# Kernel tuning notes

Hardware: AMD Instinct MI355X
Metric: run time of the kernel (lower is better)

Reference implementation:

```python
import jax, jax.numpy as jnp
import numpy as np
from jax import lax

B, T, HID, H, DK, DV, K = 2, 2048, 1024, 16, 64, 64, 4
SCALE = float(DK) ** -0.5
EPS = 1e-5


def setup_inputs() -> dict:
    key = jax.random.key(0)
    ks = jax.random.split(key, 12)
    n = lambda k, sh, s=0.02: (jax.random.normal(k, sh, jnp.float32) * s)
    return {
        "x": jax.random.normal(ks[0], (B, T, HID), jnp.float32),
        "Wq": n(ks[1], (H * DK, HID)),
        "Wk": n(ks[2], (H * DK, HID)),
        "Wv": n(ks[3], (H * DV, HID)),
        "Wa": n(ks[4], (H * DV, HID)), "ba": jnp.zeros((H * DV,), jnp.float32),
        "Wb": n(ks[5], (H, HID)), "bb": jnp.zeros((H,), jnp.float32),
        "Wg": n(ks[6], (H * DV, HID)),
        "Wo": n(ks[7], (HID, H * DV)),
        "qcw": n(ks[8], (H * DK, 1, K), 0.3), "qcb": jnp.zeros((H * DK,), jnp.float32),
        "kcw": n(ks[9], (H * DK, 1, K), 0.3), "kcb": jnp.zeros((H * DK,), jnp.float32),
        "vcw": n(ks[10], (H * DV, 1, K), 0.3), "vcb": jnp.zeros((H * DV,), jnp.float32),
        "ln_w": jnp.ones((DV,), jnp.float32), "ln_b": jnp.zeros((DV,), jnp.float32),
    }


def _causal_dwconv_silu(z, w, b):
    # z: [B,T,C], w: [C,1,K] depthwise. Conv1d(padding=K-1) then slice[:T] == causal left-pad.
    zc = z.transpose(0, 2, 1)  # [B,C,T]
    y = lax.conv_general_dilated(zc, w, (1,), [(K - 1, 0)],
                                 dimension_numbers=("NCH", "OIH", "NCH"),
                                 feature_group_count=zc.shape[1])
    return jax.nn.silu((y + b[None, :, None]).transpose(0, 2, 1))


def reference(x, Wq, Wk, Wv, Wa, ba, Wb, bb, Wg, Wo,
              qcw, qcb, kcw, kcb, vcw, vcb, ln_w, ln_b):
    Bb, Tt, _ = x.shape
    q = _causal_dwconv_silu(x @ Wq.T, qcw, qcb).reshape(Bb, Tt, H, DK)
    k = _causal_dwconv_silu(x @ Wk.T, kcw, kcb).reshape(Bb, Tt, H, DK) * SCALE
    v = _causal_dwconv_silu(x @ Wv.T, vcw, vcb).reshape(Bb, Tt, H, DV)
    a = jax.nn.sigmoid(x @ Wa.T + ba).reshape(Bb, Tt, H, DV)
    beta = jax.nn.sigmoid(x @ Wb.T + bb)  # [B,T,H]

    def step(S, inp):
        qt, kt, vt, at, bt = inp  # qt/kt: [B,H,DK], vt/at: [B,H,DV], bt: [B,H]
        err = jnp.einsum("bhij,bhj->bhi", S, kt) - vt          # S@k - v
        S = at[..., None] * S - bt[..., None, None] * (err[..., None] * kt[:, :, None, :])
        o = jnp.einsum("bhij,bhj->bhi", S, qt)                 # S@q
        return S, o

    xs = tuple(jnp.moveaxis(t, 1, 0) for t in (q, k, v, a, beta))  # time-leading
    S0 = jnp.zeros((Bb, H, DV, DK), x.dtype)
    _, o = lax.scan(step, S0, xs)
    o = jnp.moveaxis(o, 0, 1)  # [B,T,H,DV]

    mu = o.mean(-1, keepdims=True)
    var = ((o - mu) ** 2).mean(-1, keepdims=True)
    o = (o - mu) / jnp.sqrt(var + EPS) * ln_w + ln_b

    g = jax.nn.sigmoid(x @ Wg.T).reshape(Bb, Tt, H, DV)
    o = (o * g).reshape(Bb, Tt, H * DV)
    return o @ Wo.T
```

## Files before the change

### kernel.cpp

```cpp
#include <hip/hip_runtime.h>
#include <hip/hip_bf16.h>
#include <cstdint>


using bf16 = __hip_bfloat16;
typedef __bf16 bf16x8 __attribute__((ext_vector_type(8)));
typedef __bf16 bf16x4v __attribute__((ext_vector_type(4)));
typedef float f32x4 __attribute__((ext_vector_type(4)));
typedef float f32x2 __attribute__((ext_vector_type(2)));
typedef unsigned int u32x4 __attribute__((ext_vector_type(4)));
typedef unsigned int u32x2 __attribute__((ext_vector_type(2)));

__device__ __forceinline__ __bf16 cvt_bf16(float f) {
  __hip_bfloat16 h = (__hip_bfloat16)f;
  return *reinterpret_cast<__bf16*>(&h);
}
__device__ __forceinline__ void async_copy16(const void* g, void* l) {
  __builtin_amdgcn_global_load_lds((const __attribute__((address_space(1))) void*)g,
                                   (__attribute__((address_space(3))) void*)l,
                                   16, 0, 0);
}
__device__ __forceinline__ float bcf(unsigned int u) { return __builtin_bit_cast(float, u); }
template <int CTRL>
__device__ __forceinline__ float dpp_f(float x) {
  int y = __builtin_amdgcn_update_dpp(0, __builtin_bit_cast(int, x), CTRL, 0xF, 0xF, true);
  return __builtin_bit_cast(float, y);
}

__global__ __launch_bounds__(256) void cvtw_kernel(
    const float* __restrict__ x, const float* __restrict__ Wq,
    const float* __restrict__ Wk, const float* __restrict__ Wv,
    const float* __restrict__ Wa, const float* __restrict__ Wg,
    const float* __restrict__ Wo, bf16* __restrict__ xb,
    bf16* __restrict__ w4b, bf16* __restrict__ wgb, bf16* __restrict__ wob)
{
  int blk = blockIdx.x;
  const float* src;
  __bf16* dst;
  size_t off;
  if (blk < 4096) {
    src = x; dst = (__bf16*)xb;
    off = (size_t)blk * 1024 + threadIdx.x * 4;
  } else if (blk < 8192) {
    int wb = blk - 4096;
    int wi = wb >> 10;
    src = (wi == 0) ? Wq : (wi == 1) ? Wk : (wi == 2) ? Wv : Wa;
    dst = (__bf16*)w4b + (size_t)wi * 1024 * 1024;
    off = (size_t)(wb & 1023) * 1024 + threadIdx.x * 4;
  } else if (blk < 9216) {
    src = Wg; dst = (__bf16*)wgb;
    off = (size_t)(blk - 8192) * 1024 + threadIdx.x * 4;
  } else {
    src = Wo; dst = (__bf16*)wob;
    off = (size_t)(blk - 9216) * 1024 + threadIdx.x * 4;
  }
  float4 f = *(const float4*)(src + off);
  bf16x4v t;
  t[0] = cvt_bf16(f.x); t[1] = cvt_bf16(f.y); t[2] = cvt_bf16(f.z); t[3] = cvt_bf16(f.w);
  *(bf16x4v*)(dst + off) = t;
}

template <int MODE, bool A_FP32>
__global__ __launch_bounds__(256) void gemm_bt(
    const void* __restrict__ Av, const float* __restrict__ Bt,
    const float* __restrict__ bias, float* __restrict__ Cf, bf16* __restrict__ Cb,
    int M, int N, int K)
{
  __shared__ __align__(16) __bf16 As[128 * 32];
  __shared__ __align__(16) __bf16 Bs[128 * 32];

  const int tid  = threadIdx.x;
  const int lane = tid & 63;
  const int wave = tid >> 6;
  const int tile_m = blockIdx.y * 128;
  const int tile_n = blockIdx.x * 128;
  const int wm = (wave >> 1) * 64;
  const int wn = (wave & 1) * 64;

  const int srow = lane >> 2;
  const int scol = (lane & 3) * 8;

  f32x4 acc[4][4];
#pragma unroll
  for (int i = 0; i < 4; ++i)
#pragma unroll
    for (int j = 0; j < 4; ++j) acc[i][j] = {0.f, 0.f, 0.f, 0.f};

  for (int k0 = 0; k0 < K; k0 += 32) {
    float4 b0[2], b1[2], a0[2], a1[2];
#pragma unroll
    for (int s = 0; s < 2; ++s) {
      int brow = tile_n + s * 64 + wave * 16 + srow;
      if (brow > N - 1) brow = N - 1;
      const float* bp = Bt + (size_t)brow * K + k0 + scol;
      b0[s] = *(const float4*)bp;
      b1[s] = *(const float4*)(bp + 4);
      if (A_FP32) {
        int arow = tile_m + s * 64 + wave * 16 + srow;
        const float* ap = (const float*)Av + (size_t)arow * K + k0 + scol;
        a0[s] = *(const float4*)ap;
        a1[s] = *(const float4*)(ap + 4);
      }
    }
    __syncthreads();
#pragma unroll
    for (int s = 0; s < 2; ++s) {
      if (!A_FP32) {
        int arow = tile_m + s * 64 + wave * 16 + srow;
        async_copy16((const __bf16*)Av + (size_t)arow * K + k0 + scol,
                     &As[(s * 64 + wave * 16 + srow) * 32 + scol]);
      } else {
        bf16x8 ua;
        ua[0] = cvt_bf16(a0[s].x); ua[1] = cvt_bf16(a0[s].y);
        ua[2] = cvt_bf16(a0[s].z); ua[3] = cvt_bf16(a0[s].w);
        ua[4] = cvt_bf16(a1[s].x); ua[5] = cvt_bf16(a1[s].y);
        ua[6] = cvt_bf16(a1[s].z); ua[7] = cvt_bf16(a1[s].w);
        *(bf16x8*)&As[(s * 64 + wave * 16 + srow) * 32 + scol] = ua;
      }
      bf16x8 u;
      u[0] = cvt_bf16(b0[s].x); u[1] = cvt_bf16(b0[s].y);
      u[2] = cvt_bf16(b0[s].z); u[3] = cvt_bf16(b0[s].w);
      u[4] = cvt_bf16(b1[s].x); u[5] = cvt_bf16(b1[s].y);
      u[6] = cvt_bf16(b1[s].z); u[7] = cvt_bf16(b1[s].w);
      *(bf16x8*)&Bs[(s * 64 + wave * 16 + srow) * 32 + scol] = u;
    }
    __syncthreads();

    bf16x8 af[4], bfr[4];
#pragma unroll
    for (int i = 0; i < 4; ++i)
      af[i] = *(const bf16x8*)&As[(wm + i * 16 + (lane & 15)) * 32 + (lane >> 4) * 8];
#pragma unroll
    for (int j = 0; j < 4; ++j)
      bfr[j] = *(const bf16x8*)&Bs[(wn + j * 16 + (lane & 15)) * 32 + (lane >> 4) * 8];

#pragma unroll
    for (int i = 0; i < 4; ++i)
#pragma unroll
      for (int j = 0; j < 4; ++j)
        acc[i][j] = __builtin_amdgcn_mfma_f32_16x16x32_bf16(af[i], bfr[j], acc[i][j], 0, 0, 0);
  }

#pragma unroll
  for (int i = 0; i < 4; ++i) {
#pragma unroll
    for (int j = 0; j < 4; ++j) {
#pragma unroll
      for (int r = 0; r < 4; ++r) {
        int gm = tile_m + wm + i * 16 + (lane >> 4) * 4 + r;
        int gn = tile_n + wn + j * 16 + (lane & 15);
        if (gn < N) {
          float val = acc[i][j][r];
          if (MODE == 3 || MODE == 5) {
            float bv = bias ? bias[gn] : 0.f;
            val = 1.f / (1.f + __expf(-(val + bv)));
          }
          if (MODE == 4)      Cf[(size_t)gm * N + gn] = val;
          else if (MODE == 5) Cf[(size_t)gn * M + gm] = val;
          else                Cb[(size_t)gm * N + gn] = (bf16)val;
        }
      }
    }
  }
}

__global__ __launch_bounds__(256) void gemm_bb(
    const bf16* __restrict__ A, const bf16* __restrict__ Bw,
    float* __restrict__ C)
{
  __shared__ __align__(16) __bf16 As[128 * 32];
  __shared__ __align__(16) __bf16 Bs[128 * 32];

  const int tid  = threadIdx.x;
  const int lane = tid & 63;
  const int wave = tid >> 6;
  const int tile_m = blockIdx.y * 128;
  const int tile_n = blockIdx.x * 128;
  const int wm = (wave >> 1) * 64;
  const int wn = (wave & 1) * 64;
  const int srow = lane >> 2;
  const int scol = (lane & 3) * 8;

  f32x4 acc[4][4];
#pragma unroll
  for (int i = 0; i < 4; ++i)
#pragma unroll
    for (int j = 0; j < 4; ++j) acc[i][j] = {0.f, 0.f, 0.f, 0.f};

  for (int k0 = 0; k0 < 1024; k0 += 32) {
    __syncthreads();
#pragma unroll
    for (int s = 0; s < 2; ++s) {
      int arow = tile_m + s * 64 + wave * 16 + srow;
      async_copy16((const __bf16*)A + (size_t)arow * 1024 + k0 + scol,
                   &As[(s * 64 + wave * 16 + srow) * 32 + scol]);
      int brow = tile_n + s * 64 + wave * 16 + srow;
      async_copy16((const __bf16*)Bw + (size_t)brow * 1024 + k0 + scol,
                   &Bs[(s * 64 + wave * 16 + srow) * 32 + scol]);
    }
    __syncthreads();

    bf16x8 af[4], bfr[4];
#pragma unroll
    for (int i = 0; i < 4; ++i)
      af[i] = *(const bf16x8*)&As[(wm + i * 16 + (lane & 15)) * 32 + (lane >> 4) * 8];
#pragma unroll
    for (int j = 0; j < 4; ++j)
      bfr[j] = *(const bf16x8*)&Bs[(wn + j * 16 + (lane & 15)) * 32 + (lane >> 4) * 8];

#pragma unroll
    for (int i = 0; i < 4; ++i)
#pragma unroll
      for (int j = 0; j < 4; ++j)
        acc[i][j] = __builtin_amdgcn_mfma_f32_16x16x32_bf16(af[i], bfr[j], acc[i][j], 0, 0, 0);
  }

#pragma unroll
  for (int i = 0; i < 4; ++i)
#pragma unroll
    for (int j = 0; j < 4; ++j)
#pragma unroll
      for (int r = 0; r < 4; ++r) {
        int gm = tile_m + wm + i * 16 + (lane >> 4) * 4 + r;
        int gn = tile_n + wn + j * 16 + (lane & 15);
        C[(size_t)gm * 1024 + gn] = acc[i][j][r];
      }
}

__global__ __launch_bounds__(256) void mega_gemm2(
    const bf16* __restrict__ Av, const bf16* __restrict__ W4b,
    const float* __restrict__ Wb, const float* __restrict__ bb,
    const float* __restrict__ ba, bf16* __restrict__ C4,
    float* __restrict__ betab)
{
  __shared__ __align__(16) __bf16 As[128 * 32];
  __shared__ __align__(16) __bf16 Bs[128 * 32];

  const int tid  = threadIdx.x;
  const int lane = tid & 63;
  const int wave = tid >> 6;
  const int tile_m = blockIdx.y * 128;
  const bool isbeta = (blockIdx.x >= 32);
  const int tile_n = isbeta ? 0 : blockIdx.x * 128;
  const int grp = tile_n >> 10;
  const int tnl = tile_n & 1023;
  const int wm = (wave >> 1) * 64;
  const int wn = (wave & 1) * 64;

  const int srow = lane >> 2;
  const int scol = (lane & 3) * 8;

  f32x4 acc[4][4];
#pragma unroll
  for (int i = 0; i < 4; ++i)
#pragma unroll
    for (int j = 0; j < 4; ++j) acc[i][j] = {0.f, 0.f, 0.f, 0.f};

  const __bf16* Wp = (const __bf16*)W4b + (size_t)grp * 1024 * 1024;

  for (int k0 = 0; k0 < 1024; k0 += 32) {
    float4 b0[2], b1[2];
    if (isbeta) {
#pragma unroll
      for (int s = 0; s < 2; ++s) {
        int brow = s * 64 + wave * 16 + srow;
        if (brow > 15) brow = 15;
        const float* bp = Wb + (size_t)brow * 1024 + k0 + scol;
        b0[s] = *(const float4*)bp;
        b1[s] = *(const float4*)(bp + 4);
      }
    }
    __syncthreads();
#pragma unroll
    for (int s = 0; s < 2; ++s) {
      int arow = tile_m + s * 64 + wave * 16 + srow;
      async_copy16((const __bf16*)Av + (size_t)arow * 1024 + k0 + scol,
                   &As[(s * 64 + wave * 16 + srow) * 32 + scol]);
      if (!isbeta) {
        int brow = tnl + s * 64 + wave * 16 + srow;
        async_copy16(Wp + (size_t)brow * 1024 + k0 + scol,
                     &Bs[(s * 64 + wave * 16 + srow) * 32 + scol]);
      } else {
        bf16x8 u;
        u[0] = cvt_bf16(b0[s].x); u[1] = cvt_bf16(b0[s].y);
        u[2] = cvt_bf16(b0[s].z); u[3] = cvt_bf16(b0[s].w);
        u[4] = cvt_bf16(b1[s].x); u[5] = cvt_bf16(b1[s].y);
        u[6] = cvt_bf16(b1[s].z); u[7] = cvt_bf16(b1[s].w);
        *(bf16x8*)&Bs[(s * 64 + wave * 16 + srow) * 32 + scol] = u;
      }
    }
    __syncthreads();

    bf16x8 af[4], bfr[4];
#pragma unroll
    for (int i = 0; i < 4; ++i)
      af[i] = *(const bf16x8*)&As[(wm + i * 16 + (lane & 15)) * 32 + (lane >> 4) * 8];
#pragma unroll
    for (int j = 0; j < 4; ++j)
      bfr[j] = *(const bf16x8*)&Bs[(wn + j * 16 + (lane & 15)) * 32 + (lane >> 4) * 8];

#pragma unroll
    for (int i = 0; i < 4; ++i)
#pragma unroll
      for (int j = 0; j < 4; ++j)
        acc[i][j] = __builtin_amdgcn_mfma_f32_16x16x32_bf16(af[i], bfr[j], acc[i][j], 0, 0, 0);
  }

  if (!isbeta) {
    bf16* Cp = (bf16*)((__bf16*)C4 + (size_t)grp * 4096 * 1024);
#pragma unroll
    for (int i = 0; i < 4; ++i)
#pragma unroll
      for (int j = 0; j < 4; ++j)
#pragma unroll
        for (int r = 0; r < 4; ++r) {
          int gm = tile_m + wm + i * 16 + (lane >> 4) * 4 + r;
          int col = tnl + wn + j * 16 + (lane & 15);
          float val = acc[i][j][r];
          if (grp == 3) val = 1.f / (1.f + __expf(-(val + ba[col])));
          ((__bf16*)Cp)[(size_t)gm * 1024 + col] = cvt_bf16(val);
        }
  } else {
#pragma unroll
    for (int i = 0; i < 4; ++i)
#pragma unroll
      for (int j = 0; j < 4; ++j)
#pragma unroll
        for (int r = 0; r < 4; ++r) {
          int gm = tile_m + wm + i * 16 + (lane >> 4) * 4 + r;
          int gn = wn + j * 16 + (lane & 15);
          if (gn < 16) {
            float val = 1.f / (1.f + __expf(-(acc[i][j][r] + bb[gn])));
            betab[(size_t)gn * 4096 + gm] = val;
          }
        }
  }
}

__global__ __launch_bounds__(256) void conv_silu_kernel(
    const bf16* __restrict__ z, const float* __restrict__ w,
    const float* __restrict__ bias, bf16* __restrict__ out, float scale)
{
  int idx = blockIdx.x * 256 + threadIdx.x;
  int c8 = idx & 127;
  int m  = idx >> 7;
  int t  = m & 2047;
  int c0 = c8 * 8;

  const __bf16* base = (const __bf16*)z + (size_t)m * 1024 + c0;
  const bf16x8 zzero = __builtin_bit_cast(bf16x8, (u32x4){0u, 0u, 0u, 0u});
  bf16x8 z3 = *(const bf16x8*)base;
  bf16x8 z2 = (t >= 1) ? *(const bf16x8*)(base - 1024) : zzero;
  bf16x8 z1 = (t >= 2) ? *(const bf16x8*)(base - 2048) : zzero;
  bf16x8 z0 = (t >= 3) ? *(const bf16x8*)(base - 3072) : zzero;

  const float* wp = w + c0 * 4;
  bf16x8 res;
#pragma unroll
  for (int e = 0; e < 8; ++e) {
    float4 we = *(const float4*)(wp + e * 4);
    float acc = bias[c0 + e] + (float)z3[e] * we.w;
    acc += (float)z2[e] * we.z;
    acc += (float)z1[e] * we.y;
    acc += (float)z0[e] * we.x;
    float s = acc / (1.f + __expf(-acc));
    res[e] = cvt_bf16(s * scale);
  }
  *(bf16x8*)((__bf16*)out + (size_t)m * 1024 + c0) = res;
}

__global__ __launch_bounds__(256) void kk_kernel(
    const bf16* __restrict__ k, const float* __restrict__ betab,
    float* __restrict__ G)
{
  int tid = blockIdx.x * 256 + threadIdx.x;
  int out = tid >> 2;
  int j   = tid & 3;
  int h = out >> 12;
  int m = out & 4095;
  int t = m & 2047;
  float s = 0.f;
  if (t > 0) {
    const __bf16* r1 = (const __bf16*)k + (size_t)m * 1024 + h * 64 + j * 16;
    const __bf16* r0 = r1 - 1024;
    bf16x8 a0 = *(const bf16x8*)r0;
    bf16x8 a1 = *(const bf16x8*)(r0 + 8);
    bf16x8 b0 = *(const bf16x8*)r1;
    bf16x8 b1 = *(const bf16x8*)(r1 + 8);
#pragma unroll
    for (int e = 0; e < 8; ++e)
      s += (float)a0[e] * (float)b0[e] + (float)a1[e] * (float)b1[e];
  }
  s += __shfl_xor(s, 1);
  s += __shfl_xor(s, 2);
  if (j == 0) G[out] = betab[out] * s;
}

#define SCAN_STEP(i, KN0, KN1, Q0, Q1, WV, WA, BT, GT, LAST)                  \
  {                                                                           \
    const float vr = ((i) & 1) ? bcf((WV) & 0xffff0000u) : bcf((WV) << 16);   \
    const float ar = ((i) & 1) ? bcf((WA) & 0xffff0000u) : bcf((WA) << 16);   \
    float unxt = 0.f;                                                         \
    f32x2 k2n0 = {0.f, 0.f}, k2n1 = {0.f, 0.f};                               \
    if (!(LAST)) {                                                            \
      k2n0 = unpk(KN0); k2n1 = unpk(KN1);                                     \
      f32x2 dd = S20 * k2n0; dd += S21 * k2n1;                                \
      unxt = dd[0] + dd[1];                                                   \
      unxt += dpp_f<0xB1>(unxt);  unxt += dpp_f<0x4E>(unxt);                  \
      unxt += dpp_f<0x141>(unxt); unxt += dpp_f<0x140>(unxt);                 \
    } else { Sold0 = S20; Sold1 = S21; }                                      \
    float A_ = (BT) * __builtin_fmaf(aprev, u, -vr);                          \
    cc = __builtin_fmaf(-cc, (GT), A_);                                       \
    f32x2 q20 = unpk(Q0), q21 = unpk(Q1);                                     \
    const f32x2 cc2 = {cc, cc}, arv = {ar, ar};                               \
    f32x2 oo;                                                                 \
    { f32x2 t0 = cc2 * k2c0; S20 = arv * S20 - t0; oo = S20 * q20;            \
      f32x2 t1 = cc2 * k2c1; S21 = arv * S21 - t1; oo += S21 * q21; }         \
    so[(i)][lane] = oo[0] + oo[1];                                            \
    aprev = ar;                                                               \
    if (!(LAST)) { k2c0 = k2n0; k2c1 = k2n1; u = unxt; }                      \
  }

#define LOADG(KS, QS, VS, AS, BS, GS, g)                                      \
  KS = *(const u32x4*)&skT[buf][sg][(g) * 8];                                 \
  QS = *(const u32x4*)&sqT[buf][sg][(g) * 8];                                 \
  VS = *(const unsigned int*)&svaT[buf][0][r4][(g) * 2];                      \
  AS = *(const unsigned int*)&svaT[buf][1][r4][(g) * 2];                      \
  BS = *(const f32x2*)&sbeta[c * 16 + (g) * 2];                               \
  GS = *(const f32x2*)&sG[c * 16 + (g) * 2];

__global__ __launch_bounds__(256) void scan_gemm_kernel(
    const bf16* __restrict__ q, const bf16* __restrict__ k,
    const bf16* __restrict__ v, const bf16* __restrict__ a,
    const float* __restrict__ betab, const float* __restrict__ gkk,
    bf16* __restrict__ o,
    const float* __restrict__ x, const bf16* __restrict__ Wgb,
    bf16* __restrict__ gout)
{
  __shared__ __align__(16) __bf16 skT[2][16][72];
  __shared__ __align__(16) __bf16 sqT[2][16][72];
  __shared__ __align__(16) __bf16 svaT[2][2][4][16];
  __shared__ __align__(16) float  so[16][68];
  __shared__ __align__(16) __bf16 so2[16][4];
  __shared__ float sbeta[2048];
  __shared__ float sG[2048];
  __shared__ __align__(16) __bf16 As[128 * 32];
  __shared__ __align__(16) __bf16 Bs[128 * 32];

  if (blockIdx.x >= 512) {
    const int gb   = blockIdx.x - 512;
    const int tid  = threadIdx.x;
    const int lane = tid & 63;
    const int wave = tid >> 6;
    const int tile_m = (gb >> 3) * 128;
    const int tile_n = (gb & 7) * 128;
    const int wm = (wave >> 1) * 64;
    const int wn = (wave & 1) * 64;
    const int srow = lane >> 2;
    const int scol = (lane & 3) * 8;

    f32x4 acc[4][4];
#pragma unroll
    for (int i = 0; i < 4; ++i)
#pragma unroll
      for (int j = 0; j < 4; ++j) acc[i][j] = {0.f, 0.f, 0.f, 0.f};

    for (int k0 = 0; k0 < 1024; k0 += 32) {
      float4 a0[2], a1[2];
#pragma unroll
      for (int s = 0; s < 2; ++s) {
        int arow = tile_m + s * 64 + wave * 16 + srow;
        const float* ap = x + (size_t)arow * 1024 + k0 + scol;
        a0[s] = *(const float4*)ap;
        a1[s] = *(const float4*)(ap + 4);
      }
      __syncthreads();
#pragma unroll
      for (int s = 0; s < 2; ++s) {
        bf16x8 ua;
        ua[0] = cvt_bf16(a0[s].x); ua[1] = cvt_bf16(a0[s].y);
        ua[2] = cvt_bf16(a0[s].z); ua[3] = cvt_bf16(a0[s].w);
        ua[4] = cvt_bf16(a1[s].x); ua[5] = cvt_bf16(a1[s].y);
        ua[6] = cvt_bf16(a1[s].z); ua[7] = cvt_bf16(a1[s].w);
        *(bf16x8*)&As[(s * 64 + wave * 16 + srow) * 32 + scol] = ua;
        int brow = tile_n + s * 64 + wave * 16 + srow;
        async_copy16((const __bf16*)Wgb + (size_t)brow * 1024 + k0 + scol,
                     &Bs[(s * 64 + wave * 16 + srow) * 32 + scol]);
      }
      __syncthreads();

      bf16x8 af[4], bfr[4];
#pragma unroll
      for (int i = 0; i < 4; ++i)
        af[i] = *(const bf16x8*)&As[(wm + i * 16 + (lane & 15)) * 32 + (lane >> 4) * 8];
#pragma unroll
      for (int j = 0; j < 4; ++j)
        bfr[j] = *(const bf16x8*)&Bs[(wn + j * 16 + (lane & 15)) * 32 + (lane >> 4) * 8];

#pragma unroll
      for (int i = 0; i < 4; ++i)
#pragma unroll
        for (int j = 0; j < 4; ++j)
          acc[i][j] = __builtin_amdgcn_mfma_f32_16x16x32_bf16(af[i], bfr[j], acc[i][j], 0, 0, 0);
    }

#pragma unroll
    for (int i = 0; i < 4; ++i)
#pragma unroll
      for (int j = 0; j < 4; ++j)
#pragma unroll
        for (int r = 0; r < 4; ++r) {
          int gm = tile_m + wm + i * 16 + (lane >> 4) * 4 + r;
          int gn = tile_n + wn + j * 16 + (lane & 15);
          float val = 1.f / (1.f + __expf(-acc[i][j][r]));
          gout[(size_t)gm * 1024 + gn] = (bf16)val;
        }
    return;
  }

  if (threadIdx.x >= 64) return;

  const int blk = blockIdx.x;
  const int qd = blk >> 5;
  const int bh = blk & 31;
  const int b = bh >> 4, h = bh & 15;
  const int lane = threadIdx.x;
  const int r4 = lane >> 4;
  const int sg = lane & 15;

  {
    const float* bp = betab + (size_t)h * 4096 + b * 2048;
    const float* gp = gkk   + (size_t)h * 4096 + b * 2048;
    for (int t = lane; t < 2048; t += 64) { sbeta[t] = bp[t]; sG[t] = gp[t]; }
  }

  const size_t bkq = (size_t)b * 2048 * 1024 + h * 64;
  const size_t bva = bkq + qd * 4;
  const __bf16* kp = (const __bf16*)k;
  const __bf16* qp = (const __bf16*)q;

  const int g_st = lane >> 3;
  const int g_cg = (lane & 7) * 8;
  const int sgp  = (lane & 7) * 2;
  const int va_vh = (lane >> 4) & 1;
  const int va_st = lane & 15;

  bf16x8 pk0, pk1, pq0, pq1;
  bf16x4v pva;
  auto fetch = [&](int t0) {
    int st0 = t0 + g_st, st1 = t0 + 8 + g_st;
    pk0 = *(const bf16x8*)(kp + bkq + (size_t)st0 * 1024 + g_cg);
    pk1 = *(const bf16x8*)(kp + bkq + (size_t)st1 * 1024 + g_cg);
    pq0 = *(const bf16x8*)(qp + bkq + (size_t)st0 * 1024 + g_cg);
    pq1 = *(const bf16x8*)(qp + bkq + (size_t)st1 * 1024 + g_cg);
    if (lane < 32) {
      const __bf16* src = va_vh ? (const __bf16*)a : (const __bf16*)v;
      pva = *(const bf16x4v*)(src + bva + (size_t)(t0 + va_st) * 1024);
    }
  };
  auto commit = [&](int cb) {
    {
      u32x4 wk = __builtin_bit_cast(u32x4, pk0);
      u32x4 wq = __builtin_bit_cast(u32x4, pq0);
      u32x2 lo, hi;
      lo[0] = wk[0]; lo[1] = wk[1]; hi[0] = wk[2]; hi[1] = wk[3];
      *(u32x2*)&skT[cb][sgp][g_st * 4]     = lo;
      *(u32x2*)&skT[cb][sgp + 1][g_st * 4] = hi;
      lo[0] = wq[0]; lo[1] = wq[1]; hi[0] = wq[2]; hi[1] = wq[3];
      *(u32x2*)&sqT[cb][sgp][g_st * 4]     = lo;
      *(u32x2*)&sqT[cb][sgp + 1][g_st * 4] = hi;
    }
    {
      u32x4 wk = __builtin_bit_cast(u32x4, pk1);
      u32x4 wq = __builtin_bit_cast(u32x4, pq1);
      u32x2 lo, hi;
      lo[0] = wk[0]; lo[1] = wk[1]; hi[0] = wk[2]; hi[1] = wk[3];
      *(u32x2*)&skT[cb][sgp][(8 + g_st) * 4]     = lo;
      *(u32x2*)&skT[cb][sgp + 1][(8 + g_st) * 4] = hi;
      lo[0] = wq[0]; lo[1] = wq[1]; hi[0] = wq[2]; hi[1] = wq[3];
      *(u32x2*)&sqT[cb][sgp][(8 + g_st) * 4]     = lo;
      *(u32x2*)&sqT[cb][sgp + 1][(8 + g_st) * 4] = hi;
    }
    if (lane < 32) {
#pragma unroll
      for (int r = 0; r < 4; ++r) svaT[cb][va_vh][r][va_st] = pva[r];
    }
  };

  fetch(0); commit(0);

  f32x2 S20 = {0.f, 0.f}, S21 = {0.f, 0.f};
  f32x2 Sold0 = {0.f, 0.f}, Sold1 = {0.f, 0.f};
  float u = 0.f, cc = 0.f, aprev = 0.f;

  auto unpk = [&](unsigned int w) -> f32x2 {
    f32x2 r; r[0] = bcf(w << 16); r[1] = bcf(w & 0xffff0000u); return r;
  };

  for (int c = 0; c < 128; ++c) {
    const int buf = c & 1;
    const bool hasNext = (c + 1 < 128);

    if (hasNext) fetch((c + 1) * 16);

    u32x4 kA, qA, kB, qB, kC, qC;
    unsigned int vA, aA, vB, aB, vC, aC;
    f32x2 bA, gA, bB, gB, bC, gC;

    LOADG(kA, qA, vA, aA, bA, gA, 0)
    LOADG(kB, qB, vB, aB, bB, gB, 1)
    LOADG(kC, qC, vC, aC, bC, gC, 2)

    f32x2 k2c0 = unpk(kA[0]);
    f32x2 k2c1 = unpk(kA[1]);
    {
      f32x2 dd = Sold0 * k2c0;
      dd += Sold1 * k2c1;
      float un = dd[0] + dd[1];
      un += dpp_f<0xB1>(un);
      un += dpp_f<0x4E>(un);
      un += dpp_f<0x141>(un);
      un += dpp_f<0x140>(un);
      u = un;
    }

    SCAN_STEP(0,  kA[2], kA[3], qA[0], qA[1], vA, aA, bA[0], gA[0], false)
    SCAN_STEP(1,  kB[0], kB[1], qA[2], qA[3], vA, aA, bA[1], gA[1], false)
    LOADG(kA, qA, vA, aA, bA, gA, 3)
    SCAN_STEP(2,  kB[2], kB[3], qB[0], qB[1], vB, aB, bB[0], gB[0], false)
    SCAN_STEP(3,  kC[0], kC[1], qB[2], qB[3], vB, aB, bB[1], gB[1], false)
    LOADG(kB, qB, vB, aB, bB, gB, 4)
    SCAN_STEP(4,  kC[2], kC[3], qC[0], qC[1], vC, aC, bC[0], gC[0], false)
    SCAN_STEP(5,  kA[0], kA[1], qC[2], qC[3], vC, aC, bC[1], gC[1], false)
    LOADG(kC, qC, vC, aC, bC, gC, 5)
    SCAN_STEP(6,  kA[2], kA[3], qA[0], qA[1], vA, aA, bA[0], gA[0], false)
    SCAN_STEP(7,  kB[0], kB[1], qA[2], qA[3], vA, aA, bA[1], gA[1], false)
    LOADG(kA, qA, vA, aA, bA, gA, 6)
    SCAN_STEP(8,  kB[2], kB[3], qB[0], qB[1], vB, aB, bB[0], gB[0], false)
    SCAN_STEP(9,  kC[0], kC[1], qB[2], qB[3], vB, aB, bB[1], gB[1], false)
    LOADG(kB, qB, vB, aB, bB, gB, 7)
    SCAN_STEP(10, kC[2], kC[3], qC[0], qC[1], vC, aC, bC[0], gC[0], false)
    SCAN_STEP(11, kA[0], kA[1], qC[2], qC[3], vC, aC, bC[1], gC[1], false)
    SCAN_STEP(12, kA[2], kA[3], qA[0], qA[1], vA, aA, bA[0], gA[0], false)
    SCAN_STEP(13, kB[0], kB[1], qA[2], qA[3], vA, aA, bA[1], gA[1], false)
    SCAN_STEP(14, kB[2], kB[3], qB[0], qB[1], vB, aB, bB[0], gB[0], false)
    SCAN_STEP(15, kB[2], kB[3], qB[2], qB[3], vB, aB, bB[1], gB[1], true)

    {
      int st = lane >> 2, rr = lane & 3;
      float4 A0 = *(const float4*)&so[st][rr * 16];
      float4 A1 = *(const float4*)&so[st][rr * 16 + 4];
      float4 A2 = *(const float4*)&so[st][rr * 16 + 8];
      float4 A3 = *(const float4*)&so[st][rr * 16 + 12];
      float s = (((A0.x + A0.y) + (A0.z + A0.w)) + ((A1.x + A1.y) + (A1.z + A1.w)))
              + (((A2.x + A2.y) + (A2.z + A2.w)) + ((A3.x + A3.y) + (A3.z + A3.w)));
      so2[st][rr] = cvt_bf16(s);
    }
    if (lane < 16)
      *(bf16x4v*)((__bf16*)o + bva + (size_t)(c * 16 + lane) * 1024) =
          *(const bf16x4v*)&so2[lane][0];

    if (hasNext) commit(buf ^ 1);
  }
}

__global__ __launch_bounds__(256) void ln_gate_kernel(
    const bf16* __restrict__ o, const bf16* __restrict__ g,
    const float* __restrict__ lnw, const float* __restrict__ lnb,
    bf16* __restrict__ out)
{
  int row = blockIdx.x * 4 + (threadIdx.x >> 6);
  int lane = threadIdx.x & 63;
  size_t idx = (size_t)row * 64 + lane;
  float xv = (float)o[idx];
  float mu = xv;
#pragma unroll
  for (int s = 1; s < 64; s <<= 1) mu += __shfl_xor(mu, s);
  mu *= (1.f / 64.f);
  float d = xv - mu;
  float vv = d * d;
#pragma unroll
  for (int s = 1; s < 64; s <<= 1) vv += __shfl_xor(vv, s);
  vv *= (1.f / 64.f);
  float y = d * rsqrtf(vv + 1e-5f) * lnw[lane] + lnb[lane];
  y *= (float)g[idx];
  out[idx] = (bf16)y;
}

extern "C" void kernel_launch(void* const* d_in, const int* in_sizes, int n_in,
                              void* d_out, int out_size, void* d_ws, size_t ws_size,
                              hipStream_t stream)
{
  const float* x   = (const float*)d_in[0];
  const float* Wq  = (const float*)d_in[1];
  const float* Wk  = (const float*)d_in[2];
  const float* Wv  = (const float*)d_in[3];
  const float* Wa  = (const float*)d_in[4];
  const float* ba  = (const float*)d_in[5];
  const float* Wb  = (const float*)d_in[6];
  const float* bb  = (const float*)d_in[7];
  const float* Wg  = (const float*)d_in[8];
  const float* Wo  = (const float*)d_in[9];
  const float* qcw = (const float*)d_in[10];
  const float* qcb = (const float*)d_in[11];
  const float* kcw = (const float*)d_in[12];
  const float* kcb = (const float*)d_in[13];
  const float* vcw = (const float*)d_in[14];
  const float* vcb = (const float*)d_in[15];
  const float* lnw = (const float*)d_in[16];
  const float* lnb = (const float*)d_in[17];

  const int M = 4096, HID = 1024;
  const size_t PLANE = (size_t)M * HID;
  const size_t PB = PLANE * sizeof(bf16);

  char* ws = (char*)d_ws;
  float* outf = (float*)d_out;
  const bool rich = (ws_size >= 5 * PB + 1024);

  dim3 blk(256);
  dim3 g8(8, 32);
  int nconv = (int)((size_t)M * 128 / 256);

  if (rich) {
    bf16* P0 = (bf16*)(ws);
    bf16* P1 = (bf16*)(ws + PB);
    bf16* P2 = (bf16*)(ws + 2 * PB);
    bf16* P3 = (bf16*)(ws + 3 * PB);
    bf16* P4 = (bf16*)(ws + 4 * PB);
    bf16*  xb    = (bf16*)d_out;
    bf16*  W4b   = (bf16*)((char*)d_out + 8 * 1024 * 1024);
    bf16*  Kb    = xb;
    bf16*  Qb    = W4b;
    float* betab = (float*)P4;
    float* gkk   = (float*)((char*)P4 + 256 * 1024);
    bf16*  Wgb   = (bf16*)((char*)P4 + 1024 * 1024);
    bf16*  Wob   = (bf16*)((char*)P4 + 3 * 1024 * 1024);

    cvtw_kernel<<<10240, blk, 0, stream>>>(x, Wq, Wk, Wv, Wa, Wg, Wo,
                                           xb, W4b, Wgb, Wob);
    mega_gemm2<<<dim3(33, 32), blk, 0, stream>>>(xb, W4b, Wb, bb, ba, P0, betab);
    conv_silu_kernel<<<nconv, blk, 0, stream>>>(P0, qcw, qcb, Qb, 1.f);
    conv_silu_kernel<<<nconv, blk, 0, stream>>>(P1, kcw, kcb, Kb, 0.125f);
    conv_silu_kernel<<<nconv, blk, 0, stream>>>(P2, vcw, vcb, P1, 1.f);
    kk_kernel<<<1024, blk, 0, stream>>>(Kb, betab, gkk);
    scan_gemm_kernel<<<768, blk, 0, stream>>>(Qb, Kb, P1, P3, betab, gkk, P0,
                                              x, Wgb, P2);
    ln_gate_kernel<<<M * 16 / 4, blk, 0, stream>>>(P0, P2, lnw, lnb, P1);
    gemm_bb<<<g8, blk, 0, stream>>>(P1, Wob, outf);
  } else {
    bf16* P  = (bf16*)(ws);
    bf16* qb = (bf16*)(ws + PB);
    bf16* kb = (bf16*)(ws + 2 * PB);
    bf16* vb = (bf16*)(ws + 3 * PB);
    float* betab = (float*)d_out;
    float* gkk   = (float*)((char*)d_out + 256 * 1024);
    bf16*  ob    = (bf16*)((char*)d_out + 8 * 1024 * 1024);

    gemm_bt<2, true><<<g8, blk, 0, stream>>>(x, Wq, nullptr, nullptr, P, M, HID, HID);
    conv_silu_kernel<<<nconv, blk, 0, stream>>>(P, qcw, qcb, qb, 1.f);
    gemm_bt<2, true><<<g8, blk, 0, stream>>>(x, Wk, nullptr, nullptr, P, M, HID, HID);
    conv_silu_kernel<<<nconv, blk, 0, stream>>>(P, kcw, kcb, kb, 0.125f);
    gemm_bt<2, true><<<g8, blk, 0, stream>>>(x, Wv, nullptr, nullptr, P, M, HID, HID);
    conv_silu_kernel<<<nconv, blk, 0, stream>>>(P, vcw, vcb, vb, 1.f);
    gemm_bt<3, true><<<g8, blk, 0, stream>>>(x, Wa, ba, nullptr, P, M, HID, HID);
    gemm_bt<5, true><<<dim3(1, 32), blk, 0, stream>>>(x, Wb, bb, betab, nullptr, M, 16, HID);
    kk_kernel<<<1024, blk, 0, stream>>>(kb, betab, gkk);
    scan_gemm_kernel<<<512, blk, 0, stream>>>(qb, kb, vb, P, betab, gkk, ob,
                                              x, nullptr, nullptr);
    gemm_bt<3, true><<<g8, blk, 0, stream>>>(x, Wg, nullptr, nullptr, qb, M, HID, HID);
    ln_gate_kernel<<<M * 16 / 4, blk, 0, stream>>>(ob, qb, lnw, lnb, kb);
    gemm_bt<4, false><<<g8, blk, 0, stream>>>(kb, Wo, nullptr, outf, nullptr, M, HID, HID);
  }
}
```

Baseline: 460.8 us.

## Fuse LayerNorm+gate into output GEMM and merge conv/kk kernel launches

The output GEMM now loads o and g directly, computes per-head LayerNorm and the sigmoid-gate multiply in registers, and writes the normalized A tile into shared memory, removing the separate ln_gate kernel and its intermediate buffer. The three conv_silu launches and kk_kernel are merged into two launches (q/k conv together, v conv plus kk). This cuts launch count and global round trips. In exchange, each GEMM column-tile block recomputes the LayerNorm for its rows (8x redundant), and the A operand is no longer loaded asynchronously.

```diff
diff --git a/kernel.cpp b/kernel.cpp
--- a/kernel.cpp
+++ b/kernel.cpp
@@ -164,12 +164,14 @@
   }
 }
 
-__global__ __launch_bounds__(256) void gemm_bb(
-    const bf16* __restrict__ A, const bf16* __restrict__ Bw,
-    float* __restrict__ C)
-{
-  __shared__ __align__(16) __bf16 As[128 * 32];
+__global__ __launch_bounds__(256) void gemm_bb_ln(
+    const bf16* __restrict__ o, const bf16* __restrict__ g,
+    const float* __restrict__ lnw, const float* __restrict__ lnb,
+    const bf16* __restrict__ Bw, float* __restrict__ C)
+{
+  __shared__ __align__(16) __bf16 As2[128][72];
   __shared__ __align__(16) __bf16 Bs[128 * 32];
+  __shared__ float sW[64], sB[64];
 
   const int tid  = threadIdx.x;
   const int lane = tid & 63;
@@ -180,6 +182,10 @@
   const int wn = (wave & 1) * 64;
   const int srow = lane >> 2;
   const int scol = (lane & 3) * 8;
+  const int rl = tid >> 1;
+  const int half = tid & 1;
+
+  if (tid < 64) { sW[tid] = lnw[tid]; sB[tid] = lnb[tid]; }
 
   f32x4 acc[4][4];
 #pragma unroll
@@ -187,32 +193,76 @@
 #pragma unroll
     for (int j = 0; j < 4; ++j) acc[i][j] = {0.f, 0.f, 0.f, 0.f};
 
-  for (int k0 = 0; k0 < 1024; k0 += 32) {
+  for (int h = 0; h < 16; ++h) {
     __syncthreads();
-#pragma unroll
-    for (int s = 0; s < 2; ++s) {
-      int arow = tile_m + s * 64 + wave * 16 + srow;
-      async_copy16((const __bf16*)A + (size_t)arow * 1024 + k0 + scol,
-                   &As[(s * 64 + wave * 16 + srow) * 32 + scol]);
-      int brow = tile_n + s * 64 + wave * 16 + srow;
-      async_copy16((const __bf16*)Bw + (size_t)brow * 1024 + k0 + scol,
-                   &Bs[(s * 64 + wave * 16 + srow) * 32 + scol]);
-    }
-    __syncthreads();
-
-    bf16x8 af[4], bfr[4];
-#pragma unroll
-    for (int i = 0; i < 4; ++i)
-      af[i] = *(const bf16x8*)&As[(wm + i * 16 + (lane & 15)) * 32 + (lane >> 4) * 8];
-#pragma unroll
-    for (int j = 0; j < 4; ++j)
-      bfr[j] = *(const bf16x8*)&Bs[(wn + j * 16 + (lane & 15)) * 32 + (lane >> 4) * 8];
-
-#pragma unroll
-    for (int i = 0; i < 4; ++i)
+
+    const __bf16* op = (const __bf16*)o + (size_t)(tile_m + rl) * 1024 + h * 64 + half * 32;
+    const __bf16* gp = (const __bf16*)g + (size_t)(tile_m + rl) * 1024 + h * 64 + half * 32;
+    bf16x8 ov0 = *(const bf16x8*)(op);
+    bf16x8 ov1 = *(const bf16x8*)(op + 8);
+    bf16x8 ov2 = *(const bf16x8*)(op + 16);
+    bf16x8 ov3 = *(const bf16x8*)(op + 24);
+    bf16x8 gv0 = *(const bf16x8*)(gp);
+    bf16x8 gv1 = *(const bf16x8*)(gp + 8);
+    bf16x8 gv2 = *(const bf16x8*)(gp + 16);
+    bf16x8 gv3 = *(const bf16x8*)(gp + 24);
+
+    float sum = 0.f;
+#pragma unroll
+    for (int e = 0; e < 8; ++e)
+      sum += (float)ov0[e] + (float)ov1[e] + (float)ov2[e] + (float)ov3[e];
+    sum += __shfl_xor(sum, 1);
+    float mu = sum * (1.f / 64.f);
+    float vv = 0.f;
+#pragma unroll
+    for (int e = 0; e < 8; ++e) {
+      float d0 = (float)ov0[e] - mu, d1 = (float)ov1[e] - mu;
+      float d2 = (float)ov2[e] - mu, d3 = (float)ov3[e] - mu;
+      vv += d0 * d0 + d1 * d1 + d2 * d2 + d3 * d3;
+    }
+    vv += __shfl_xor(vv, 1);
+    float rstd = rsqrtf(vv * (1.f / 64.f) + 1e-5f);
+
+    bf16x8 res0, res1, res2, res3;
+#pragma unroll
+    for (int e = 0; e < 8; ++e) {
+      int c0 = half * 32 + e;
+      res0[e] = cvt_bf16((((float)ov0[e] - mu) * rstd * sW[c0] + sB[c0]) * (float)gv0[e]);
+      res1[e] = cvt_bf16((((float)ov1[e] - mu) * rstd * sW[c0 + 8] + sB[c0 + 8]) * (float)gv1[e]);
+      res2[e] = cvt_bf16((((float)ov2[e] - mu) * rstd * sW[c0 + 16] + sB[c0 + 16]) * (float)gv2[e]);
+      res3[e] = cvt_bf16((((float)ov3[e] - mu) * rstd * sW[c0 + 24] + sB[c0 + 24]) * (float)gv3[e]);
+    }
+    *(bf16x8*)&As2[rl][half * 32 + 0]  = res0;
+    *(bf16x8*)&As2[rl][half * 32 + 8]  = res1;
+    *(bf16x8*)&As2[rl][half * 32 + 16] = res2;
+    *(bf16x8*)&As2[rl][half * 32 + 24] = res3;
+
+#pragma unroll
+    for (int sub = 0; sub < 2; ++sub) {
+      if (sub) __syncthreads();
+      int k0 = h * 64 + sub * 32;
+#pragma unroll
+      for (int s = 0; s < 2; ++s) {
+        int brow = tile_n + s * 64 + wave * 16 + srow;
+        async_copy16((const __bf16*)Bw + (size_t)brow * 1024 + k0 + scol,
+                     &Bs[(s * 64 + wave * 16 + srow) * 32 + scol]);
+      }
+      __syncthreads();
+
+      bf16x8 af[4], bfr[4];
+#pragma unroll
+      for (int i = 0; i < 4; ++i)
+        af[i] = *(const bf16x8*)&As2[wm + i * 16 + (lane & 15)][(lane >> 4) * 8 + sub * 32];
 #pragma unroll
       for (int j = 0; j < 4; ++j)
-        acc[i][j] = __builtin_amdgcn_mfma_f32_16x16x32_bf16(af[i], bfr[j], acc[i][j], 0, 0, 0);
+        bfr[j] = *(const bf16x8*)&Bs[(wn + j * 16 + (lane & 15)) * 32 + (lane >> 4) * 8];
+
+#pragma unroll
+      for (int i = 0; i < 4; ++i)
+#pragma unroll
+        for (int j = 0; j < 4; ++j)
+          acc[i][j] = __builtin_amdgcn_mfma_f32_16x16x32_bf16(af[i], bfr[j], acc[i][j], 0, 0, 0);
+    }
   }
 
 #pragma unroll
@@ -337,11 +387,10 @@
   }
 }
 
-__global__ __launch_bounds__(256) void conv_silu_kernel(
-    const bf16* __restrict__ z, const float* __restrict__ w,
+__device__ __forceinline__ void conv_body(
+    int idx, const bf16* __restrict__ z, const float* __restrict__ w,
     const float* __restrict__ bias, bf16* __restrict__ out, float scale)
 {
-  int idx = blockIdx.x * 256 + threadIdx.x;
   int c8 = idx & 127;
   int m  = idx >> 7;
   int t  = m & 2047;
@@ -367,6 +416,59 @@
     res[e] = cvt_bf16(s * scale);
   }
   *(bf16x8*)((__bf16*)out + (size_t)m * 1024 + c0) = res;
+}
+
+__global__ __launch_bounds__(256) void conv_silu_kernel(
+    const bf16* __restrict__ z, const float* __restrict__ w,
+    const float* __restrict__ bias, bf16* __restrict__ out, float scale)
+{
+  conv_body(blockIdx.x * 256 + threadIdx.x, z, w, bias, out, scale);
+}
+
+__global__ __launch_bounds__(256) void conv2_kernel(
+    const bf16* __restrict__ zq, const bf16* __restrict__ zk,
+    const float* __restrict__ qcw, const float* __restrict__ qcb,
+    const float* __restrict__ kcw, const float* __restrict__ kcb,
+    bf16* __restrict__ oq, bf16* __restrict__ ok)
+{
+  int sec = blockIdx.x >> 11;
+  int bx  = blockIdx.x & 2047;
+  int idx = bx * 256 + threadIdx.x;
+  if (sec == 0) conv_body(idx, zq, qcw, qcb, oq, 1.f);
+  else          conv_body(idx, zk, kcw, kcb, ok, 0.125f);
+}
+
+__global__ __launch_bounds__(256) void convv_kk_kernel(
+    const bf16* __restrict__ zv, const float* __restrict__ vcw,
+    const float* __restrict__ vcb, bf16* __restrict__ ov,
+    const bf16* __restrict__ k, const float* __restrict__ betab,
+    float* __restrict__ G)
+{
+  if (blockIdx.x < 2048) {
+    conv_body(blockIdx.x * 256 + threadIdx.x, zv, vcw, vcb, ov, 1.f);
+    return;
+  }
+  int gtid = (blockIdx.x - 2048) * 256 + threadIdx.x;
+  int out = gtid >> 2;
+  int j   = gtid & 3;
+  int h = out >> 12;
+  int m = out & 4095;
+  int t = m & 2047;
+  float s = 0.f;
+  if (t > 0) {
+    const __bf16* r1 = (const __bf16*)k + (size_t)m * 1024 + h * 64 + j * 16;
+    const __bf16* r0 = r1 - 1024;
+    bf16x8 a0 = *(const bf16x8*)r0;
+    bf16x8 a1 = *(const bf16x8*)(r0 + 8);
+    bf16x8 b0 = *(const bf16x8*)r1;
+    bf16x8 b1 = *(const bf16x8*)(r1 + 8);
+#pragma unroll
+    for (int e = 0; e < 8; ++e)
+      s += (float)a0[e] * (float)b0[e] + (float)a1[e] * (float)b1[e];
+  }
+  s += __shfl_xor(s, 1);
+  s += __shfl_xor(s, 2);
+  if (j == 0) G[out] = betab[out] * s;
 }
 
 __global__ __launch_bounds__(256) void kk_kernel(
@@ -740,14 +842,11 @@
     cvtw_kernel<<<10240, blk, 0, stream>>>(x, Wq, Wk, Wv, Wa, Wg, Wo,
                                            xb, W4b, Wgb, Wob);
     mega_gemm2<<<dim3(33, 32), blk, 0, stream>>>(xb, W4b, Wb, bb, ba, P0, betab);
-    conv_silu_kernel<<<nconv, blk, 0, stream>>>(P0, qcw, qcb, Qb, 1.f);
-    conv_silu_kernel<<<nconv, blk, 0, stream>>>(P1, kcw, kcb, Kb, 0.125f);
-    conv_silu_kernel<<<nconv, blk, 0, stream>>>(P2, vcw, vcb, P1, 1.f);
-    kk_kernel<<<1024, blk, 0, stream>>>(Kb, betab, gkk);
+    conv2_kernel<<<4096, blk, 0, stream>>>(P0, P1, qcw, qcb, kcw, kcb, Qb, Kb);
+    convv_kk_kernel<<<3072, blk, 0, stream>>>(P2, vcw, vcb, P1, Kb, betab, gkk);
     scan_gemm_kernel<<<768, blk, 0, stream>>>(Qb, Kb, P1, P3, betab, gkk, P0,
                                               x, Wgb, P2);
-    ln_gate_kernel<<<M * 16 / 4, blk, 0, stream>>>(P0, P2, lnw, lnb, P1);
-    gemm_bb<<<g8, blk, 0, stream>>>(P1, Wob, outf);
+    gemm_bb_ln<<<g8, blk, 0, stream>>>(P0, P2, lnw, lnb, Wob, outf);
   } else {
     bf16* P  = (bf16*)(ws);
     bf16* qb = (bf16*)(ws + PB);
```

New measurement: 457.4 us. Within noise of the previous version (-0.7%).
